# Optimization experiments

Hardware: AMD Instinct MI355X
Metric: run time of the kernel (lower is better)

The kernel has to match this reference:

```python
import jax, jax.numpy as jnp
import numpy as np

NUM_AGENTS = 64
IN_FEATURES = 512
OUT_FEATURES = 512
BATCH = 2048


def setup_inputs() -> dict:
    key = jax.random.key(0)
    k1, k2, k3, k4 = jax.random.split(key, 4)
    which_agents = jax.random.randint(k1, (BATCH,), 0, NUM_AGENTS, dtype=jnp.int64 if jax.config.jax_enable_x64 else jnp.int32)
    x = jax.random.normal(k2, (BATCH, IN_FEATURES), dtype=jnp.float32)
    # kaiming_uniform_(a=sqrt(5)) -> bound = sqrt(6 / ((1 + 5) * fan_in)) = 1/sqrt(fan_in)
    bound_w = 1.0 / np.sqrt(IN_FEATURES)
    weight = jax.random.uniform(k3, (NUM_AGENTS, OUT_FEATURES, IN_FEATURES), jnp.float32, -bound_w, bound_w)
    bound_b = 1.0 / np.sqrt(IN_FEATURES)
    bias = jax.random.uniform(k4, (NUM_AGENTS, OUT_FEATURES), jnp.float32, -bound_b, bound_b)
    return {"which_agents": which_agents, "input": x, "weight": weight, "bias": bias}


def reference(which_agents, input, weight, bias):
    # weight[which_agents]: [B, out, in]; batched matvec with input [B, in]
    w = weight[which_agents]          # [B, O, I]
    b = bias[which_agents]            # [B, O]
    return jnp.einsum('boi,bi->bo', w, input) + b
```

## Files before the change

### kernel.cpp

```cpp
#include <hip/hip_runtime.h>


constexpr int BATCH  = 2048;
constexpr int NAGENT = 64;
constexpr int IN_F   = 512;
constexpr int OUT_F  = 512;

constexpr int BN  = 64;
constexpr int MCH = 64;
constexpr int XS  = IN_F + 8;

typedef __attribute__((ext_vector_type(8))) short short8;
typedef __attribute__((ext_vector_type(4))) float f32x4;
typedef __attribute__((ext_vector_type(4))) unsigned int u32x4;

__device__ inline unsigned rnd_bf(float f) {
  unsigned u = __float_as_uint(f);
  return u + 0x7FFFu + ((u >> 16) & 1u);
}
__device__ inline unsigned pk_bf(float lo, float hi) {
  return (rnd_bf(lo) >> 16) | (rnd_bf(hi) & 0xFFFF0000u);
}

__global__ __launch_bounds__(256, 2) void agent_linear_v4(
    const int*   __restrict__ which,
    const float* __restrict__ x,
    const float* __restrict__ weight,
    const float* __restrict__ bias,
    float*       __restrict__ out) {
  const int tid   = threadIdx.x;
  const int lane  = tid & 63;
  const int wid   = tid >> 6;
  const int agent = blockIdx.y;
  const int obase = blockIdx.x * BN;

  __shared__ int wsum_s[4];
  __shared__ int rowlist_s[BATCH];
  __shared__ __align__(16) unsigned short Xs[MCH * XS];

  int vals[8];
  {
    const int4* w4 = (const int4*)which;
    int4 v0 = w4[tid * 2];
    int4 v1 = w4[tid * 2 + 1];
    vals[0] = v0.x; vals[1] = v0.y; vals[2] = v0.z; vals[3] = v0.w;
    vals[4] = v1.x; vals[5] = v1.y; vals[6] = v1.z; vals[7] = v1.w;
  }
  int lc = 0;
#pragma unroll
  for (int u = 0; u < 8; ++u) lc += (vals[u] == agent) ? 1 : 0;
  int s = lc;
#pragma unroll
  for (int off = 1; off < 64; off <<= 1) {
    int t = __shfl_up(s, off);
    if (lane >= off) s += t;
  }
  if (lane == 63) wsum_s[wid] = s;
  __syncthreads();
  int base = 0, count = 0;
#pragma unroll
  for (int w = 0; w < 4; ++w) {
    int ws = wsum_s[w];
    if (w < wid) base += ws;
    count += ws;
  }
  {
    int pos = base + s - lc;
#pragma unroll
    for (int u = 0; u < 8; ++u)
      if (vals[u] == agent) rowlist_s[pos++] = tid * 8 + u;
  }
  __syncthreads();

  const int nl = lane & 15;
  const int kq = lane >> 4;

  const float* wp = weight + ((size_t)(agent * OUT_F + obase + wid * 16 + nl)) * IN_F + kq * 8;
  const float  bv = bias[agent * OUT_F + obase + wid * 16 + nl];

  for (int m0 = 0; m0 < count; m0 += MCH) {
    const int mcount = min(MCH, count - m0);
    __syncthreads();

#pragma unroll 4
    for (int t = 0; t < 32; ++t) {
      int idx = t * 256 + tid;
      int r   = idx >> 7;
      int c4  = idx & 127;
      if (r < mcount) {
        float4 xv = *(const float4*)(x + (size_t)rowlist_s[m0 + r] * IN_F + c4 * 4);
        uint2 w2;
        w2.x = pk_bf(xv.x, xv.y);
        w2.y = pk_bf(xv.z, xv.w);
        *(uint2*)&Xs[r * XS + c4 * 4] = w2;
      }
    }
    __syncthreads();

    f32x4 acc[4] = {{0.f,0.f,0.f,0.f},{0.f,0.f,0.f,0.f},
                    {0.f,0.f,0.f,0.f},{0.f,0.f,0.f,0.f}};
    float4 pa[4], pb[4];
#pragma unroll
    for (int p = 0; p < 4; ++p) {
      pa[p] = *(const float4*)(wp + p * 32);
      pb[p] = *(const float4*)(wp + p * 32 + 4);
    }
#pragma unroll
    for (int k = 0; k < 16; ++k) {
      float4 c0 = pa[k & 3], c1 = pb[k & 3];
      if (k + 4 < 16) {
        pa[k & 3] = *(const float4*)(wp + (k + 4) * 32);
        pb[k & 3] = *(const float4*)(wp + (k + 4) * 32 + 4);
      }
      u32x4 q;
      q[0] = pk_bf(c0.x, c0.y); q[1] = pk_bf(c0.z, c0.w);
      q[2] = pk_bf(c1.x, c1.y); q[3] = pk_bf(c1.z, c1.w);
      short8 bf = __builtin_bit_cast(short8, q);
#pragma unroll
      for (int i = 0; i < 4; ++i) {
        short8 af = *(const short8*)&Xs[(i * 16 + nl) * XS + k * 32 + kq * 8];
        acc[i] = __builtin_amdgcn_mfma_f32_16x16x32_bf16(af, bf, acc[i], 0, 0, 0);
      }
    }

#pragma unroll
    for (int i = 0; i < 4; ++i) {
#pragma unroll
      for (int r = 0; r < 4; ++r) {
        int m = i * 16 + kq * 4 + r;
        if (m < mcount) {
          out[(size_t)rowlist_s[m0 + m] * OUT_F + obase + wid * 16 + nl] =
              acc[i][r] + bv;
        }
      }
    }
  }
}

extern "C" void kernel_launch(void* const* d_in, const int* in_sizes, int n_in,
                              void* d_out, int out_size, void* d_ws, size_t ws_size,
                              hipStream_t stream) {
  const int*   which = (const int*)d_in[0];
  const float* x     = (const float*)d_in[1];
  const float* w     = (const float*)d_in[2];
  const float* b     = (const float*)d_in[3];
  float*       out   = (float*)d_out;

  dim3 grid(OUT_F / BN, NAGENT);
  agent_linear_v4<<<grid, dim3(256), 0, stream>>>(which, x, w, b, out);
}
```

Baseline: 115.0 us.

## Split K across blocks with atomics and move row bucketing to a prologue kernel

A separate prologue kernel now builds per-agent row lists in workspace and initializes the output with the bias. The main kernel splits the input dimension into two halves across grid z, using smaller M chunks and LDS, and accumulates partial results with atomicAdd. The aim is more blocks, higher occupancy and less redundant per-block bucketing of the agent indices. The cost is an extra launch, atomic traffic on every output, and re-reading the row list from global memory.

```diff
diff --git a/kernel.cpp b/kernel.cpp
--- a/kernel.cpp
+++ b/kernel.cpp
@@ -7,8 +7,12 @@
 constexpr int OUT_F  = 512;
 
 constexpr int BN  = 64;
-constexpr int MCH = 64;
-constexpr int XS  = IN_F + 8;
+constexpr int KH  = 256;
+constexpr int MCH = 32;
+constexpr int XS  = KH + 8;
+
+#define WS_CNT(ws)  ((int*)(ws))
+#define WS_ROW(ws)  ((int*)((char*)(ws) + 1024))
 
 typedef __attribute__((ext_vector_type(8))) short short8;
 typedef __attribute__((ext_vector_type(4))) float f32x4;
@@ -22,73 +26,94 @@
   return (rnd_bf(lo) >> 16) | (rnd_bf(hi) & 0xFFFF0000u);
 }
 
-__global__ __launch_bounds__(256, 2) void agent_linear_v4(
+__global__ __launch_bounds__(256) void prologue(
     const int*   __restrict__ which,
+    const float* __restrict__ bias,
+    float*       __restrict__ out,
+    int*         __restrict__ wscnt,
+    int*         __restrict__ wsrow) {
+  const int bid = blockIdx.x;
+  const int tid = threadIdx.x;
+  if (bid < NAGENT) {
+    const int agent = bid;
+    const int lane = tid & 63, wid = tid >> 6;
+    __shared__ int wsum_s[4];
+    int vals[8];
+    {
+      const int4* w4 = (const int4*)which;
+      int4 v0 = w4[tid * 2];
+      int4 v1 = w4[tid * 2 + 1];
+      vals[0] = v0.x; vals[1] = v0.y; vals[2] = v0.z; vals[3] = v0.w;
+      vals[4] = v1.x; vals[5] = v1.y; vals[6] = v1.z; vals[7] = v1.w;
+    }
+    int lc = 0;
+#pragma unroll
+    for (int u = 0; u < 8; ++u) lc += (vals[u] == agent) ? 1 : 0;
+    int s = lc;
+#pragma unroll
+    for (int off = 1; off < 64; off <<= 1) {
+      int t = __shfl_up(s, off);
+      if (lane >= off) s += t;
+    }
+    if (lane == 63) wsum_s[wid] = s;
+    __syncthreads();
+    int base = 0, count = 0;
+#pragma unroll
+    for (int w = 0; w < 4; ++w) {
+      int ws = wsum_s[w];
+      if (w < wid) base += ws;
+      count += ws;
+    }
+    int pos = base + s - lc;
+#pragma unroll
+    for (int u = 0; u < 8; ++u)
+      if (vals[u] == agent) wsrow[agent * BATCH + pos++] = tid * 8 + u;
+    if (tid == 0) wscnt[agent] = count;
+  } else {
+    const int row = (bid - NAGENT) * 32 + (tid >> 3);
+    const int a   = which[row];
+    const float4* bp = (const float4*)(bias + (size_t)a * OUT_F);
+    float4*       op = (float4*)(out + (size_t)row * OUT_F);
+#pragma unroll
+    for (int c = tid & 7; c < OUT_F / 4; c += 8) op[c] = bp[c];
+  }
+}
+
+__global__ __launch_bounds__(256, 8) void agent_linear_v5(
     const float* __restrict__ x,
     const float* __restrict__ weight,
-    const float* __restrict__ bias,
-    float*       __restrict__ out) {
+    float*       __restrict__ out,
+    const int*   __restrict__ wscnt,
+    const int*   __restrict__ wsrow) {
   const int tid   = threadIdx.x;
   const int lane  = tid & 63;
   const int wid   = tid >> 6;
+  const int nt    = blockIdx.x;
   const int agent = blockIdx.y;
-  const int obase = blockIdx.x * BN;
+  const int kh    = blockIdx.z;
+  const int obase = nt * BN;
+  const int count = wscnt[agent];
+  const int* rl   = wsrow + agent * BATCH;
 
-  __shared__ int wsum_s[4];
-  __shared__ int rowlist_s[BATCH];
   __shared__ __align__(16) unsigned short Xs[MCH * XS];
-
-  int vals[8];
-  {
-    const int4* w4 = (const int4*)which;
-    int4 v0 = w4[tid * 2];
-    int4 v1 = w4[tid * 2 + 1];
-    vals[0] = v0.x; vals[1] = v0.y; vals[2] = v0.z; vals[3] = v0.w;
-    vals[4] = v1.x; vals[5] = v1.y; vals[6] = v1.z; vals[7] = v1.w;
-  }
-  int lc = 0;
-#pragma unroll
-  for (int u = 0; u < 8; ++u) lc += (vals[u] == agent) ? 1 : 0;
-  int s = lc;
-#pragma unroll
-  for (int off = 1; off < 64; off <<= 1) {
-    int t = __shfl_up(s, off);
-    if (lane >= off) s += t;
-  }
-  if (lane == 63) wsum_s[wid] = s;
-  __syncthreads();
-  int base = 0, count = 0;
-#pragma unroll
-  for (int w = 0; w < 4; ++w) {
-    int ws = wsum_s[w];
-    if (w < wid) base += ws;
-    count += ws;
-  }
-  {
-    int pos = base + s - lc;
-#pragma unroll
-    for (int u = 0; u < 8; ++u)
-      if (vals[u] == agent) rowlist_s[pos++] = tid * 8 + u;
-  }
-  __syncthreads();
 
   const int nl = lane & 15;
   const int kq = lane >> 4;
 
-  const float* wp = weight + ((size_t)(agent * OUT_F + obase + wid * 16 + nl)) * IN_F + kq * 8;
-  const float  bv = bias[agent * OUT_F + obase + wid * 16 + nl];
+  const float* wp = weight + ((size_t)(agent * OUT_F + obase + wid * 16 + nl)) * IN_F
+                  + kh * KH + kq * 8;
 
   for (int m0 = 0; m0 < count; m0 += MCH) {
     const int mcount = min(MCH, count - m0);
     __syncthreads();
 
-#pragma unroll 4
-    for (int t = 0; t < 32; ++t) {
+#pragma unroll
+    for (int t = 0; t < 8; ++t) {
       int idx = t * 256 + tid;
-      int r   = idx >> 7;
-      int c4  = idx & 127;
+      int r   = idx >> 6;
+      int c4  = idx & 63;
       if (r < mcount) {
-        float4 xv = *(const float4*)(x + (size_t)rowlist_s[m0 + r] * IN_F + c4 * 4);
+        float4 xv = *(const float4*)(x + (size_t)rl[m0 + r] * IN_F + kh * KH + c4 * 4);
         uint2 w2;
         w2.x = pk_bf(xv.x, xv.y);
         w2.y = pk_bf(xv.z, xv.w);
@@ -97,40 +122,36 @@
     }
     __syncthreads();
 
-    f32x4 acc[4] = {{0.f,0.f,0.f,0.f},{0.f,0.f,0.f,0.f},
-                    {0.f,0.f,0.f,0.f},{0.f,0.f,0.f,0.f}};
-    float4 pa[4], pb[4];
+    f32x4 acc[2] = {{0.f, 0.f, 0.f, 0.f}, {0.f, 0.f, 0.f, 0.f}};
+    float4 pa[2], pb[2];
+    pa[0] = *(const float4*)(wp);      pb[0] = *(const float4*)(wp + 4);
+    pa[1] = *(const float4*)(wp + 32); pb[1] = *(const float4*)(wp + 36);
 #pragma unroll
-    for (int p = 0; p < 4; ++p) {
-      pa[p] = *(const float4*)(wp + p * 32);
-      pb[p] = *(const float4*)(wp + p * 32 + 4);
-    }
-#pragma unroll
-    for (int k = 0; k < 16; ++k) {
-      float4 c0 = pa[k & 3], c1 = pb[k & 3];
-      if (k + 4 < 16) {
-        pa[k & 3] = *(const float4*)(wp + (k + 4) * 32);
-        pb[k & 3] = *(const float4*)(wp + (k + 4) * 32 + 4);
+    for (int k = 0; k < 8; ++k) {
+      float4 c0 = pa[k & 1], c1 = pb[k & 1];
+      if (k + 2 < 8) {
+        pa[k & 1] = *(const float4*)(wp + (k + 2) * 32);
+        pb[k & 1] = *(const float4*)(wp + (k + 2) * 32 + 4);
       }
       u32x4 q;
       q[0] = pk_bf(c0.x, c0.y); q[1] = pk_bf(c0.z, c0.w);
       q[2] = pk_bf(c1.x, c1.y); q[3] = pk_bf(c1.z, c1.w);
       short8 bf = __builtin_bit_cast(short8, q);
 #pragma unroll
-      for (int i = 0; i < 4; ++i) {
+      for (int i = 0; i < 2; ++i) {
         short8 af = *(const short8*)&Xs[(i * 16 + nl) * XS + k * 32 + kq * 8];
         acc[i] = __builtin_amdgcn_mfma_f32_16x16x32_bf16(af, bf, acc[i], 0, 0, 0);
       }
     }
 
 #pragma unroll
-    for (int i = 0; i < 4; ++i) {
+    for (int i = 0; i < 2; ++i) {
 #pragma unroll
       for (int r = 0; r < 4; ++r) {
         int m = i * 16 + kq * 4 + r;
         if (m < mcount) {
-          out[(size_t)rowlist_s[m0 + m] * OUT_F + obase + wid * 16 + nl] =
-              acc[i][r] + bv;
+          atomicAdd(out + (size_t)rl[m0 + m] * OUT_F + obase + wid * 16 + nl,
+                    acc[i][r]);
         }
       }
     }
@@ -145,7 +166,9 @@
   const float* w     = (const float*)d_in[2];
   const float* b     = (const float*)d_in[3];
   float*       out   = (float*)d_out;
+  int*         cnt   = WS_CNT(d_ws);
+  int*         row   = WS_ROW(d_ws);
 
-  dim3 grid(OUT_F / BN, NAGENT);
-  agent_linear_v4<<<grid, dim3(256), 0, stream>>>(which, x, w, b, out);
+  prologue<<<dim3(128), dim3(256), 0, stream>>>(which, b, out, cnt, row);
+  agent_linear_v5<<<dim3(8, 64, 2), dim3(256), 0, stream>>>(x, w, out, cnt, row);
 }
```

Measured after the change: 143.0 us. +24.4%, slower.

## Stage bf16 weight slices in double-buffered LDS and keep X rows in registers

Applied to the files above, without the earlier changes.

Swaps the roles of the operands. Each wave now loads its own 16 gathered input rows straight from global memory into bf16 register fragments. The 16-column weight groups are converted once per block and staged through a double-buffered shared-memory buffer that all four waves share. This removes the redundant per-wave weight conversion and the large X shared-memory tile, but it reloads the weights for every 64-row chunk and leaves waves idle when fewer than 64 rows are assigned to an agent.

```diff
diff --git a/kernel.cpp b/kernel.cpp
--- a/kernel.cpp
+++ b/kernel.cpp
@@ -6,9 +6,12 @@
 constexpr int IN_F   = 512;
 constexpr int OUT_F  = 512;
 
-constexpr int BN  = 64;
-constexpr int MCH = 64;
-constexpr int XS  = IN_F + 8;
+constexpr int BN    = 64;
+constexpr int GR    = 16;
+constexpr int NG    = BN / GR;
+constexpr int MCH   = 64;
+constexpr int SLICE = 260;
+constexpr int WBUF  = 16 * SLICE;
 
 typedef __attribute__((ext_vector_type(8))) short short8;
 typedef __attribute__((ext_vector_type(4))) float f32x4;
@@ -22,7 +25,7 @@
   return (rnd_bf(lo) >> 16) | (rnd_bf(hi) & 0xFFFF0000u);
 }
 
-__global__ __launch_bounds__(256, 2) void agent_linear_v4(
+__global__ __launch_bounds__(256, 2) void agent_linear_v6(
     const int*   __restrict__ which,
     const float* __restrict__ x,
     const float* __restrict__ weight,
@@ -30,13 +33,13 @@
     float*       __restrict__ out) {
   const int tid   = threadIdx.x;
   const int lane  = tid & 63;
-  const int wid   = tid >> 6;
+  const int wv    = tid >> 6;
   const int agent = blockIdx.y;
   const int obase = blockIdx.x * BN;
 
   __shared__ int wsum_s[4];
   __shared__ int rowlist_s[BATCH];
-  __shared__ __align__(16) unsigned short Xs[MCH * XS];
+  __shared__ __align__(16) unsigned Wb[2][WBUF];
 
   int vals[8];
   {
@@ -55,13 +58,13 @@
     int t = __shfl_up(s, off);
     if (lane >= off) s += t;
   }
-  if (lane == 63) wsum_s[wid] = s;
+  if (lane == 63) wsum_s[wv] = s;
   __syncthreads();
   int base = 0, count = 0;
 #pragma unroll
   for (int w = 0; w < 4; ++w) {
     int ws = wsum_s[w];
-    if (w < wid) base += ws;
+    if (w < wv) base += ws;
     count += ws;
   }
   {
@@ -75,64 +78,88 @@
   const int nl = lane & 15;
   const int kq = lane >> 4;
 
-  const float* wp = weight + ((size_t)(agent * OUT_F + obase + wid * 16 + nl)) * IN_F + kq * 8;
-  const float  bv = bias[agent * OUT_F + obase + wid * 16 + nl];
+  float bv[NG];
+#pragma unroll
+  for (int g = 0; g < NG; ++g)
+    bv[g] = bias[agent * OUT_F + obase + g * 16 + nl];
+
+  const float* wblk = weight + ((size_t)agent * OUT_F + obase) * IN_F;
+  const float* wthr = wblk + tid * 4;
+
+  int wdest[8];
+#pragma unroll
+  for (int j = 0; j < 8; ++j) {
+    int off = j * 1024 + tid * 4;
+    int r = off >> 9, kk = off & 511;
+    int i = kk >> 5, q = (kk >> 3) & 3, h = (kk & 4) >> 1;
+    wdest[j] = i * SLICE + (q * 16 + r) * 4 + h;
+  }
 
   for (int m0 = 0; m0 < count; m0 += MCH) {
     const int mcount = min(MCH, count - m0);
-    __syncthreads();
+    const bool active = (wv * 16 < mcount);
 
-#pragma unroll 4
-    for (int t = 0; t < 32; ++t) {
-      int idx = t * 256 + tid;
-      int r   = idx >> 7;
-      int c4  = idx & 127;
-      if (r < mcount) {
-        float4 xv = *(const float4*)(x + (size_t)rowlist_s[m0 + r] * IN_F + c4 * 4);
-        uint2 w2;
-        w2.x = pk_bf(xv.x, xv.y);
-        w2.y = pk_bf(xv.z, xv.w);
-        *(uint2*)&Xs[r * XS + c4 * 4] = w2;
-      }
-    }
-    __syncthreads();
+    float4 wst[8];
+#pragma unroll
+    for (int j = 0; j < 8; ++j) wst[j] = *(const float4*)(wthr + j * 1024);
 
-    f32x4 acc[4] = {{0.f,0.f,0.f,0.f},{0.f,0.f,0.f,0.f},
-                    {0.f,0.f,0.f,0.f},{0.f,0.f,0.f,0.f}};
-    float4 pa[4], pb[4];
+    short8 af[16];
+    if (active) {
+      int mr = m0 + wv * 16 + nl;
+      int myrow = rowlist_s[mr < count ? mr : m0];
+      const float* xr = x + (size_t)myrow * IN_F + kq * 8;
 #pragma unroll
-    for (int p = 0; p < 4; ++p) {
-      pa[p] = *(const float4*)(wp + p * 32);
-      pb[p] = *(const float4*)(wp + p * 32 + 4);
-    }
-#pragma unroll
-    for (int k = 0; k < 16; ++k) {
-      float4 c0 = pa[k & 3], c1 = pb[k & 3];
-      if (k + 4 < 16) {
-        pa[k & 3] = *(const float4*)(wp + (k + 4) * 32);
-        pb[k & 3] = *(const float4*)(wp + (k + 4) * 32 + 4);
-      }
-      u32x4 q;
-      q[0] = pk_bf(c0.x, c0.y); q[1] = pk_bf(c0.z, c0.w);
-      q[2] = pk_bf(c1.x, c1.y); q[3] = pk_bf(c1.z, c1.w);
-      short8 bf = __builtin_bit_cast(short8, q);
-#pragma unroll
-      for (int i = 0; i < 4; ++i) {
-        short8 af = *(const short8*)&Xs[(i * 16 + nl) * XS + k * 32 + kq * 8];
-        acc[i] = __builtin_amdgcn_mfma_f32_16x16x32_bf16(af, bf, acc[i], 0, 0, 0);
+      for (int i = 0; i < 16; ++i) {
+        float4 a0 = *(const float4*)(xr + i * 32);
+        float4 a1 = *(const float4*)(xr + i * 32 + 4);
+        u32x4 uu;
+        uu[0] = pk_bf(a0.x, a0.y); uu[1] = pk_bf(a0.z, a0.w);
+        uu[2] = pk_bf(a1.x, a1.y); uu[3] = pk_bf(a1.z, a1.w);
+        af[i] = __builtin_bit_cast(short8, uu);
       }
     }
 
 #pragma unroll
-    for (int i = 0; i < 4; ++i) {
+    for (int j = 0; j < 8; ++j) {
+      uint2 p;
+      p.x = pk_bf(wst[j].x, wst[j].y);
+      p.y = pk_bf(wst[j].z, wst[j].w);
+      *(uint2*)&Wb[0][wdest[j]] = p;
+    }
+    __syncthreads();
+
 #pragma unroll
-      for (int r = 0; r < 4; ++r) {
-        int m = i * 16 + kq * 4 + r;
-        if (m < mcount) {
-          out[(size_t)rowlist_s[m0 + m] * OUT_F + obase + wid * 16 + nl] =
-              acc[i][r] + bv;
+    for (int g = 0; g < NG; ++g) {
+      if (g + 1 < NG) {
+#pragma unroll
+        for (int j = 0; j < 8; ++j)
+          wst[j] = *(const float4*)(wthr + (g + 1) * 8192 + j * 1024);
+      }
+      if (active) {
+        f32x4 acc = {0.f, 0.f, 0.f, 0.f};
+#pragma unroll
+        for (int i = 0; i < 16; ++i) {
+          short8 bf = *(const short8*)&Wb[g & 1][i * SLICE + lane * 4];
+          acc = __builtin_amdgcn_mfma_f32_16x16x32_bf16(af[i], bf, acc, 0, 0, 0);
+        }
+#pragma unroll
+        for (int r = 0; r < 4; ++r) {
+          int m = wv * 16 + kq * 4 + r;
+          if (m < mcount)
+            out[(size_t)rowlist_s[m0 + m] * OUT_F + obase + g * 16 + nl] =
+                acc[r] + bv[g];
         }
       }
+      if (g + 1 < NG) {
+#pragma unroll
+        for (int j = 0; j < 8; ++j) {
+          uint2 p;
+          p.x = pk_bf(wst[j].x, wst[j].y);
+          p.y = pk_bf(wst[j].z, wst[j].w);
+          *(uint2*)&Wb[(g + 1) & 1][wdest[j]] = p;
+        }
+      }
+      __syncthreads();
     }
   }
 }
@@ -147,5 +174,5 @@
   float*       out   = (float*)d_out;
 
   dim3 grid(OUT_F / BN, NAGENT);
-  agent_linear_v4<<<grid, dim3(256), 0, stream>>>(which, x, w, b, out);
+  agent_linear_v6<<<grid, dim3(256), 0, stream>>>(which, x, w, b, out);
 }
```

After: 114.7 us. About the same (-0.2%).

## Split row bucketing into prologue kernel and use split-K 1024-thread blocks

Applied to the files above, without the earlier changes.

Moves the per-agent row-list construction into a separate prologue kernel that writes counts and row indices to workspace, so the main kernel no longer rescans the whole batch in every block. The main kernel uses 1024 threads, with 16 waves split four ways across the K dimension. Partial sums are reduced through shared memory, and the M chunk is halved to 32. The aim is more parallelism per block and shorter per-wave dependency chains. The cost is an extra launch, an extra barrier, and a shared-memory reduction each chunk.

```diff
diff --git a/kernel.cpp b/kernel.cpp
--- a/kernel.cpp
+++ b/kernel.cpp
@@ -7,8 +7,11 @@
 constexpr int OUT_F  = 512;
 
 constexpr int BN  = 64;
-constexpr int MCH = 64;
+constexpr int MCH = 32;
 constexpr int XS  = IN_F + 8;
+
+#define WS_CNT(ws)  ((int*)(ws))
+#define WS_ROW(ws)  ((int*)((char*)(ws) + 1024))
 
 typedef __attribute__((ext_vector_type(8))) short short8;
 typedef __attribute__((ext_vector_type(4))) float f32x4;
@@ -22,22 +25,14 @@
   return (rnd_bf(lo) >> 16) | (rnd_bf(hi) & 0xFFFF0000u);
 }
 
-__global__ __launch_bounds__(256, 2) void agent_linear_v4(
-    const int*   __restrict__ which,
-    const float* __restrict__ x,
-    const float* __restrict__ weight,
-    const float* __restrict__ bias,
-    float*       __restrict__ out) {
+__global__ __launch_bounds__(256) void prologue(
+    const int* __restrict__ which,
+    int*       __restrict__ wscnt,
+    int*       __restrict__ wsrow) {
+  const int agent = blockIdx.x;
   const int tid   = threadIdx.x;
-  const int lane  = tid & 63;
-  const int wid   = tid >> 6;
-  const int agent = blockIdx.y;
-  const int obase = blockIdx.x * BN;
-
+  const int lane  = tid & 63, wid = tid >> 6;
   __shared__ int wsum_s[4];
-  __shared__ int rowlist_s[BATCH];
-  __shared__ __align__(16) unsigned short Xs[MCH * XS];
-
   int vals[8];
   {
     const int4* w4 = (const int4*)which;
@@ -64,31 +59,51 @@
     if (w < wid) base += ws;
     count += ws;
   }
-  {
-    int pos = base + s - lc;
+  int pos = base + s - lc;
 #pragma unroll
-    for (int u = 0; u < 8; ++u)
-      if (vals[u] == agent) rowlist_s[pos++] = tid * 8 + u;
-  }
-  __syncthreads();
+  for (int u = 0; u < 8; ++u)
+    if (vals[u] == agent) wsrow[agent * BATCH + pos++] = tid * 8 + u;
+  if (tid == 0) wscnt[agent] = count;
+}
+
+__global__ __launch_bounds__(1024, 8) void agent_linear_v7(
+    const float* __restrict__ x,
+    const float* __restrict__ weight,
+    const float* __restrict__ bias,
+    float*       __restrict__ out,
+    const int*   __restrict__ wscnt,
+    const int*   __restrict__ wsrow) {
+  const int tid   = threadIdx.x;
+  const int lane  = tid & 63;
+  const int wid   = tid >> 6;
+  const int ns    = wid & 3;
+  const int ks    = wid >> 2;
+  const int agent = blockIdx.y;
+  const int obase = blockIdx.x * BN;
+  const int count = wscnt[agent];
+  const int* rl   = wsrow + agent * BATCH;
+
+  __shared__ __align__(16) unsigned short Xs[MCH * XS];
+  __shared__ float Rs[3][4][MCH][17];
 
   const int nl = lane & 15;
   const int kq = lane >> 4;
 
-  const float* wp = weight + ((size_t)(agent * OUT_F + obase + wid * 16 + nl)) * IN_F + kq * 8;
-  const float  bv = bias[agent * OUT_F + obase + wid * 16 + nl];
+  const float* wp = weight + ((size_t)(agent * OUT_F + obase + ns * 16 + nl)) * IN_F
+                  + ks * 128 + kq * 8;
+  const float  bv = bias[agent * OUT_F + obase + ns * 16 + nl];
 
   for (int m0 = 0; m0 < count; m0 += MCH) {
     const int mcount = min(MCH, count - m0);
     __syncthreads();
 
-#pragma unroll 4
-    for (int t = 0; t < 32; ++t) {
-      int idx = t * 256 + tid;
+#pragma unroll
+    for (int t = 0; t < 4; ++t) {
+      int idx = t * 1024 + tid;
       int r   = idx >> 7;
       int c4  = idx & 127;
       if (r < mcount) {
-        float4 xv = *(const float4*)(x + (size_t)rowlist_s[m0 + r] * IN_F + c4 * 4);
+        float4 xv = *(const float4*)(x + (size_t)rl[m0 + r] * IN_F + c4 * 4);
         uint2 w2;
         w2.x = pk_bf(xv.x, xv.y);
         w2.y = pk_bf(xv.z, xv.w);
@@ -97,40 +112,46 @@
     }
     __syncthreads();
 
-    f32x4 acc[4] = {{0.f,0.f,0.f,0.f},{0.f,0.f,0.f,0.f},
-                    {0.f,0.f,0.f,0.f},{0.f,0.f,0.f,0.f}};
-    float4 pa[4], pb[4];
+    float4 wv_[8];
 #pragma unroll
-    for (int p = 0; p < 4; ++p) {
-      pa[p] = *(const float4*)(wp + p * 32);
-      pb[p] = *(const float4*)(wp + p * 32 + 4);
+    for (int i = 0; i < 4; ++i) {
+      wv_[2 * i]     = *(const float4*)(wp + i * 32);
+      wv_[2 * i + 1] = *(const float4*)(wp + i * 32 + 4);
     }
+    f32x4 acc[2] = {{0.f, 0.f, 0.f, 0.f}, {0.f, 0.f, 0.f, 0.f}};
 #pragma unroll
-    for (int k = 0; k < 16; ++k) {
-      float4 c0 = pa[k & 3], c1 = pb[k & 3];
-      if (k + 4 < 16) {
-        pa[k & 3] = *(const float4*)(wp + (k + 4) * 32);
-        pb[k & 3] = *(const float4*)(wp + (k + 4) * 32 + 4);
-      }
+    for (int i = 0; i < 4; ++i) {
       u32x4 q;
-      q[0] = pk_bf(c0.x, c0.y); q[1] = pk_bf(c0.z, c0.w);
-      q[2] = pk_bf(c1.x, c1.y); q[3] = pk_bf(c1.z, c1.w);
+      q[0] = pk_bf(wv_[2 * i].x,     wv_[2 * i].y);
+      q[1] = pk_bf(wv_[2 * i].z,     wv_[2 * i].w);
+      q[2] = pk_bf(wv_[2 * i + 1].x, wv_[2 * i + 1].y);
+      q[3] = pk_bf(wv_[2 * i + 1].z, wv_[2 * i + 1].w);
       short8 bf = __builtin_bit_cast(short8, q);
 #pragma unroll
-      for (int i = 0; i < 4; ++i) {
-        short8 af = *(const short8*)&Xs[(i * 16 + nl) * XS + k * 32 + kq * 8];
-        acc[i] = __builtin_amdgcn_mfma_f32_16x16x32_bf16(af, bf, acc[i], 0, 0, 0);
+      for (int mt = 0; mt < 2; ++mt) {
+        short8 af = *(const short8*)&Xs[(mt * 16 + nl) * XS + ks * 128 + i * 32 + kq * 8];
+        acc[mt] = __builtin_amdgcn_mfma_f32_16x16x32_bf16(af, bf, acc[mt], 0, 0, 0);
       }
     }
 
+    if (ks != 0) {
 #pragma unroll
-    for (int i = 0; i < 4; ++i) {
+      for (int mt = 0; mt < 2; ++mt)
 #pragma unroll
-      for (int r = 0; r < 4; ++r) {
-        int m = i * 16 + kq * 4 + r;
-        if (m < mcount) {
-          out[(size_t)rowlist_s[m0 + m] * OUT_F + obase + wid * 16 + nl] =
-              acc[i][r] + bv;
+        for (int r = 0; r < 4; ++r)
+          Rs[ks - 1][ns][mt * 16 + kq * 4 + r][nl] = acc[mt][r];
+    }
+    __syncthreads();
+    if (ks == 0) {
+#pragma unroll
+      for (int mt = 0; mt < 2; ++mt) {
+#pragma unroll
+        for (int r = 0; r < 4; ++r) {
+          int m = mt * 16 + kq * 4 + r;
+          float v = acc[mt][r] + Rs[0][ns][m][nl] + Rs[1][ns][m][nl]
+                  + Rs[2][ns][m][nl] + bv;
+          if (m < mcount)
+            out[(size_t)rl[m0 + m] * OUT_F + obase + ns * 16 + nl] = v;
         }
       }
     }
@@ -145,7 +166,10 @@
   const float* w     = (const float*)d_in[2];
   const float* b     = (const float*)d_in[3];
   float*       out   = (float*)d_out;
+  int*         cnt   = WS_CNT(d_ws);
+  int*         row   = WS_ROW(d_ws);
 
-  dim3 grid(OUT_F / BN, NAGENT);
-  agent_linear_v4<<<grid, dim3(256), 0, stream>>>(which, x, w, b, out);
+  prologue<<<dim3(NAGENT), dim3(256), 0, stream>>>(which, cnt, row);
+  agent_linear_v7<<<dim3(OUT_F / BN, NAGENT), dim3(1024), 0, stream>>>(
+      x, w, b, out, cnt, row);
 }
```

After: 114.1 us. Within noise of the previous version (-0.8%).
